# Kernel tuning notes

Measured on AMD Instinct MI355X. Metric: run time of the kernel, lower is better.

Reference implementation:

```python
import jax, jax.numpy as jnp
import numpy as np

EPS_COS = 1e-8
EPS_SHARP = 1e-16


def setup_inputs() -> dict:
    key = jax.random.key(0)
    k1, k2, k3, k4 = jax.random.split(key, 4)
    B, H, R, C, M = 512, 512, 2048, 64, 3
    out_dim = 3 * C + 2 * M + 4  # 202
    h = jax.random.normal(k1, (B, H), dtype=jnp.float32)
    prev_w = jax.random.uniform(k2, (B, R), dtype=jnp.float32)
    prev_w = prev_w / prev_w.sum(axis=1, keepdims=True)  # valid focus distribution
    memory = jax.random.normal(k3, (B, R, C), dtype=jnp.float32)
    fc_w = jax.random.normal(k4, (out_dim, H), dtype=jnp.float32) * 0.05
    fc_b = jnp.zeros((out_dim,), dtype=jnp.float32)
    return {"h": h, "prev_w": prev_w, "memory": memory, "fc_w": fc_w, "fc_b": fc_b}


def _write_head(h, prev_w, memory, fc_w, fc_b):
    B, R, C = memory.shape
    total = fc_w.shape[0]
    shift_len = total - 3 * C - 3          # 2*max_shift + 1
    m = (shift_len - 1) // 2               # max_shift

    z = h @ fc_w.T + fc_b                  # [B, total]
    sizes = [C, 1, 1, shift_len, 1, C, C]
    offs = np.cumsum([0] + sizes)
    k     = jnp.tanh(z[:, offs[0]:offs[1]])                 # [B, C]
    beta  = jax.nn.softplus(z[:, offs[1]:offs[2]])          # [B, 1]
    g     = jax.nn.sigmoid(z[:, offs[2]:offs[3]])           # [B, 1]
    s     = jax.nn.softmax(z[:, offs[3]:offs[4]], axis=1)   # [B, 2m+1]
    gamma = jax.nn.softplus(z[:, offs[4]:offs[5]]) + 1.0    # [B, 1]
    e     = jax.nn.sigmoid(z[:, offs[5]:offs[6]])           # [B, C]
    a     = jnp.tanh(z[:, offs[6]:offs[7]])                 # [B, C]

    # content addressing: cosine similarity of k vs each memory row
    num = jnp.einsum('bc,brc->br', k, memory)
    k_n = jnp.maximum(jnp.linalg.norm(k, axis=1, keepdims=True), EPS_COS)   # [B,1]
    m_n = jnp.maximum(jnp.linalg.norm(memory, axis=2), EPS_COS)             # [B,R]
    w_c = jax.nn.softmax(beta * (num / (k_n * m_n)), axis=1)                # [B,R]

    # gated interpolation
    w_g = g * w_c + (1.0 - g) * prev_w                                      # [B,R]

    # circular shift (per-sample cross-correlation, O(B*R*(2m+1)))
    unrolled = jnp.concatenate([w_g[:, -m:], w_g, w_g[:, :m]], axis=1)      # [B, R+2m]
    windows = jnp.stack([unrolled[:, j:j + R] for j in range(2 * m + 1)], axis=1)  # [B,2m+1,R]
    w_s = jnp.einsum('bjr,bj->br', windows, s)                              # [B,R]

    # sharpen
    w_p = jnp.power(w_s, gamma)
    w = w_p / (w_p.sum(axis=1, keepdims=True) + EPS_SHARP)                  # [B,R]

    # erase + write (fused)
    wE = w[:, :, None]                                                      # [B,R,1]
    new_mem = memory * (1.0 - wE * e[:, None, :]) + wE * a[:, None, :]      # [B,R,C]
    return w, new_mem


def reference(h, prev_w, memory, fc_w, fc_b):
    return _write_head(h, prev_w, memory, fc_w, fc_b)
```

## Files before the change

### kernel.cpp

```cpp
#include <hip/hip_runtime.h>
#include <math.h>

#define BB 512
#define HH 512
#define RR 2048
#define CC 64
#define OUTD 202
#define PSTRIDE 208
#define K_OFF 0
#define E_OFF 64
#define A_OFF 128
#define S_OFF 192
#define COMBO_OFF 199
#define G_OFF 200
#define GAMMA_OFF 201

typedef float f32x4 __attribute__((ext_vector_type(4)));

__device__ __forceinline__ float softplusf_(float x) {
    return (x > 20.f) ? x : log1pf(expf(x));
}
__device__ __forceinline__ float sigmoidf_(float x) {
    return 1.f / (1.f + expf(-x));
}

__global__ __launch_bounds__(256) void params_kernel(
    const float* __restrict__ h, const float* __restrict__ fc_w,
    const float* __restrict__ fc_b, float* __restrict__ pw)
{
    __shared__ float h_sh[8][HH];
    __shared__ float z_sh[8][204];
    const int tid = threadIdx.x;
    const int b0 = blockIdx.x * 8;

    for (int idx = tid; idx < 8 * HH; idx += 256) {
        int j = idx >> 9, i = idx & 511;
        h_sh[j][i] = h[(size_t)(b0 + j) * HH + i];
    }
    __syncthreads();

    if (tid < OUTD) {
        float acc[8];
        #pragma unroll
        for (int j = 0; j < 8; ++j) acc[j] = 0.f;
        const float4* wr4 = (const float4*)(fc_w + (size_t)tid * HH);
        for (int i4 = 0; i4 < HH / 4; ++i4) {
            float4 wv = wr4[i4];
            int i = i4 * 4;
            #pragma unroll
            for (int j = 0; j < 8; ++j) {
                acc[j] = fmaf(wv.x, h_sh[j][i + 0], acc[j]);
                acc[j] = fmaf(wv.y, h_sh[j][i + 1], acc[j]);
                acc[j] = fmaf(wv.z, h_sh[j][i + 2], acc[j]);
                acc[j] = fmaf(wv.w, h_sh[j][i + 3], acc[j]);
            }
        }
        float bias = fc_b[tid];
        #pragma unroll
        for (int j = 0; j < 8; ++j) z_sh[j][tid] = acc[j] + bias;
    }
    __syncthreads();

    for (int idx = tid; idx < 8 * OUTD; idx += 256) {
        int j = idx / OUTD;
        int t = idx - j * OUTD;
        float z = z_sh[j][t];
        float* p = pw + (size_t)(b0 + j) * PSTRIDE;
        if (t < 64)            p[K_OFF + t] = tanhf(z);
        else if (t == 65)      p[G_OFF] = sigmoidf_(z);
        else if (t == 73)      p[GAMMA_OFF] = softplusf_(z) + 1.f;
        else if (t >= 74 && t < 138) p[E_OFF + (t - 74)] = sigmoidf_(z);
        else if (t >= 138)     p[A_OFF + (t - 138)] = tanhf(z);
    }
    __syncthreads();

    if (tid < 8) {
        int j = tid;
        float* p = pw + (size_t)(b0 + j) * PSTRIDE;
        float ss = 0.f;
        for (int c = 0; c < 64; ++c) {
            float kv = tanhf(z_sh[j][c]);
            ss += kv * kv;
        }
        float kn = fmaxf(sqrtf(ss), 1e-8f);
        float beta = softplusf_(z_sh[j][64]);
        p[COMBO_OFF] = beta / kn;
        float mx = -1e30f;
        for (int q = 0; q < 7; ++q) mx = fmaxf(mx, z_sh[j][66 + q]);
        float ev[7], se = 0.f;
        for (int q = 0; q < 7; ++q) { ev[q] = expf(z_sh[j][66 + q] - mx); se += ev[q]; }
        float inv = 1.f / se;
        for (int q = 0; q < 7; ++q) p[S_OFF + q] = ev[q] * inv;
    }
}

__global__ __launch_bounds__(256) void score_kernel(
    const float* __restrict__ memory, const float* __restrict__ pw,
    float* __restrict__ sc)
{
    const int tid = threadIdx.x;
    const int b = blockIdx.x >> 2;
    const int rbase = (blockIdx.x & 3) * 512;
    const int lane16 = tid & 15;
    const int rgrp = tid >> 4;
    const float* p = pw + (size_t)b * PSTRIDE;
    const float4 k4 = *(const float4*)(p + K_OFF + lane16 * 4);
    const float* memb = memory + (size_t)b * RR * CC;

    #pragma unroll 4
    for (int i = 0; i < 32; ++i) {
        int r = rbase + i * 16 + rgrp;
        float4 m4 = *(const float4*)(memb + (size_t)r * CC + lane16 * 4);
        float num = m4.x * k4.x + m4.y * k4.y + m4.z * k4.z + m4.w * k4.w;
        float ssq = m4.x * m4.x + m4.y * m4.y + m4.z * m4.z + m4.w * m4.w;
        #pragma unroll
        for (int m = 1; m < 16; m <<= 1) {
            num += __shfl_xor(num, m, 64);
            ssq += __shfl_xor(ssq, m, 64);
        }
        if (lane16 == 0)
            sc[(size_t)b * RR + r] = num / fmaxf(sqrtf(ssq), 1e-8f);
    }
}

__device__ __forceinline__ float block_reduce_sum256(float v, float* red) {
    #pragma unroll
    for (int m = 1; m < 64; m <<= 1) v += __shfl_xor(v, m, 64);
    int wid = threadIdx.x >> 6;
    if ((threadIdx.x & 63) == 0) red[wid] = v;
    __syncthreads();
    float x = red[0] + red[1] + red[2] + red[3];
    __syncthreads();
    return x;
}

__global__ __launch_bounds__(256) void weight_kernel(
    const float* __restrict__ sc, const float* __restrict__ prev_w,
    const float* __restrict__ pw, float* __restrict__ out_w)
{
    __shared__ float buf[RR];
    __shared__ float wg[RR];
    __shared__ float red[4];
    const int b = blockIdx.x;
    const int tid = threadIdx.x;
    const float* p = pw + (size_t)b * PSTRIDE;
    const float combo = p[COMBO_OFF];
    const float g = p[G_OFF];
    const float gamma = p[GAMMA_OFF];
    const float s0 = p[S_OFF + 0], s1 = p[S_OFF + 1], s2 = p[S_OFF + 2],
                s3 = p[S_OFF + 3], s4 = p[S_OFF + 4], s5 = p[S_OFF + 5],
                s6 = p[S_OFF + 6];

    float ls = 0.f;
    for (int r = tid; r < RR; r += 256) {
        float ev = expf(combo * sc[(size_t)b * RR + r]);
        buf[r] = ev;
        ls += ev;
    }
    const float se = block_reduce_sum256(ls, red);
    const float invse = 1.f / se;

    for (int r = tid; r < RR; r += 256) {
        wg[r] = g * (buf[r] * invse) + (1.f - g) * prev_w[(size_t)b * RR + r];
    }
    __syncthreads();

    float lp = 0.f;
    for (int r = tid; r < RR; r += 256) {
        float acc = s0 * wg[(r - 3) & (RR - 1)]
                  + s1 * wg[(r - 2) & (RR - 1)]
                  + s2 * wg[(r - 1) & (RR - 1)]
                  + s3 * wg[r]
                  + s4 * wg[(r + 1) & (RR - 1)]
                  + s5 * wg[(r + 2) & (RR - 1)]
                  + s6 * wg[(r + 3) & (RR - 1)];
        float wp = powf(acc, gamma);
        buf[r] = wp;
        lp += wp;
    }
    const float ps = block_reduce_sum256(lp, red);
    const float invp = 1.f / (ps + 1e-16f);

    for (int r = tid; r < RR; r += 256) {
        out_w[(size_t)b * RR + r] = buf[r] * invp;
    }
}

__global__ __launch_bounds__(256) void update_kernel(
    const float* __restrict__ memory, const float* __restrict__ w,
    const float* __restrict__ pw, float* __restrict__ out_mem)
{
    const size_t N4 = (size_t)BB * RR * CC / 4;
    const size_t stride = (size_t)2048 * 256;
    const f32x4* m4p = (const f32x4*)memory;
    f32x4* o4p = (f32x4*)out_mem;

    #pragma unroll 2
    for (size_t idx = (size_t)blockIdx.x * 256 + threadIdx.x; idx < N4;
         idx += stride) {
        int br = (int)(idx >> 4);
        int b  = (int)(idx >> 15);
        int c4 = (int)(idx & 15);
        const float* p = pw + (size_t)b * PSTRIDE;
        float wv = w[br];
        f32x4 e4 = *(const f32x4*)(p + E_OFF + c4 * 4);
        f32x4 a4 = *(const f32x4*)(p + A_OFF + c4 * 4);
        f32x4 m4 = m4p[idx];
        f32x4 o;
        o.x = m4.x * (1.f - wv * e4.x) + wv * a4.x;
        o.y = m4.y * (1.f - wv * e4.y) + wv * a4.y;
        o.z = m4.z * (1.f - wv * e4.z) + wv * a4.z;
        o.w = m4.w * (1.f - wv * e4.w) + wv * a4.w;
        __builtin_nontemporal_store(o, &o4p[idx]);
    }
}

extern "C" void kernel_launch(void* const* d_in, const int* in_sizes, int n_in,
                              void* d_out, int out_size, void* d_ws, size_t ws_size,
                              hipStream_t stream) {
    const float* h      = (const float*)d_in[0];
    const float* prev_w = (const float*)d_in[1];
    const float* memory = (const float*)d_in[2];
    const float* fc_w   = (const float*)d_in[3];
    const float* fc_b   = (const float*)d_in[4];

    float* pw      = (float*)d_ws;
    float* out_w   = (float*)d_out;
    float* out_mem = out_w + (size_t)BB * RR;
    float* sc      = out_mem;

    params_kernel<<<64, 256, 0, stream>>>(h, fc_w, fc_b, pw);
    score_kernel<<<BB * 4, 256, 0, stream>>>(memory, pw, sc);
    weight_kernel<<<BB, 256, 0, stream>>>(sc, prev_w, pw, out_w);
    update_kernel<<<2048, 256, 0, stream>>>(memory, out_w, pw, out_mem);
}
```

Before: 209.6 us.

## Move softmax exp into score kernel and reverse-order update for cache reuse

Computes exp(combo*cosine) in the score kernel so the weight kernel only sums and normalizes, and switches powf to the fast __powf. The update kernel becomes per-(batch,row-block) with reversed block order, so the memory slices most recently read by the score kernel are likely still in cache, and loads become nontemporal. It also raises the unroll factor. Risks include lower precision from the fast exp/pow intrinsics and no softmax max-subtraction, which is safe only while cosine times beta stays bounded.

```diff
diff --git a/kernel.cpp b/kernel.cpp
--- a/kernel.cpp
+++ b/kernel.cpp
@@ -105,9 +105,10 @@
     const int rgrp = tid >> 4;
     const float* p = pw + (size_t)b * PSTRIDE;
     const float4 k4 = *(const float4*)(p + K_OFF + lane16 * 4);
+    const float combo = p[COMBO_OFF];
     const float* memb = memory + (size_t)b * RR * CC;
 
-    #pragma unroll 4
+    #pragma unroll 8
     for (int i = 0; i < 32; ++i) {
         int r = rbase + i * 16 + rgrp;
         float4 m4 = *(const float4*)(memb + (size_t)r * CC + lane16 * 4);
@@ -118,8 +119,10 @@
             num += __shfl_xor(num, m, 64);
             ssq += __shfl_xor(ssq, m, 64);
         }
-        if (lane16 == 0)
-            sc[(size_t)b * RR + r] = num / fmaxf(sqrtf(ssq), 1e-8f);
+        if (lane16 == 0) {
+            float mn = fmaxf(sqrtf(ssq), 1e-8f);
+            sc[(size_t)b * RR + r] = __expf(combo * num / mn);
+        }
     }
 }
 
@@ -144,7 +147,6 @@
     const int b = blockIdx.x;
     const int tid = threadIdx.x;
     const float* p = pw + (size_t)b * PSTRIDE;
-    const float combo = p[COMBO_OFF];
     const float g = p[G_OFF];
     const float gamma = p[GAMMA_OFF];
     const float s0 = p[S_OFF + 0], s1 = p[S_OFF + 1], s2 = p[S_OFF + 2],
@@ -153,7 +155,7 @@
 
     float ls = 0.f;
     for (int r = tid; r < RR; r += 256) {
-        float ev = expf(combo * sc[(size_t)b * RR + r]);
+        float ev = sc[(size_t)b * RR + r];
         buf[r] = ev;
         ls += ev;
     }
@@ -174,7 +176,7 @@
                   + s4 * wg[(r + 1) & (RR - 1)]
                   + s5 * wg[(r + 2) & (RR - 1)]
                   + s6 * wg[(r + 3) & (RR - 1)];
-        float wp = powf(acc, gamma);
+        float wp = __powf(acc, gamma);
         buf[r] = wp;
         lp += wp;
     }
@@ -190,28 +192,31 @@
     const float* __restrict__ memory, const float* __restrict__ w,
     const float* __restrict__ pw, float* __restrict__ out_mem)
 {
-    const size_t N4 = (size_t)BB * RR * CC / 4;
-    const size_t stride = (size_t)2048 * 256;
-    const f32x4* m4p = (const f32x4*)memory;
-    f32x4* o4p = (f32x4*)out_mem;
-
-    #pragma unroll 2
-    for (size_t idx = (size_t)blockIdx.x * 256 + threadIdx.x; idx < N4;
-         idx += stride) {
-        int br = (int)(idx >> 4);
-        int b  = (int)(idx >> 15);
-        int c4 = (int)(idx & 15);
-        const float* p = pw + (size_t)b * PSTRIDE;
-        float wv = w[br];
-        f32x4 e4 = *(const f32x4*)(p + E_OFF + c4 * 4);
-        f32x4 a4 = *(const f32x4*)(p + A_OFF + c4 * 4);
-        f32x4 m4 = m4p[idx];
+    const int bid = (int)gridDim.x - 1 - (int)blockIdx.x;
+    const int b = bid >> 2;
+    const int rbase = (bid & 3) * 512;
+    const int tid = threadIdx.x;
+    const int lane16 = tid & 15;
+    const int rgrp = tid >> 4;
+    const float* p = pw + (size_t)b * PSTRIDE;
+    const f32x4 e4 = *(const f32x4*)(p + E_OFF + lane16 * 4);
+    const f32x4 a4 = *(const f32x4*)(p + A_OFF + lane16 * 4);
+    const float* memb = memory + (size_t)b * RR * CC;
+    float* omb = out_mem + (size_t)b * RR * CC;
+    const float* wb = w + (size_t)b * RR;
+
+    #pragma unroll 8
+    for (int i = 0; i < 32; ++i) {
+        int r = rbase + i * 16 + rgrp;
+        float wv = wb[r];
+        const f32x4* mp = (const f32x4*)(memb + (size_t)r * CC) + lane16;
+        f32x4 m4 = __builtin_nontemporal_load(mp);
         f32x4 o;
         o.x = m4.x * (1.f - wv * e4.x) + wv * a4.x;
         o.y = m4.y * (1.f - wv * e4.y) + wv * a4.y;
         o.z = m4.z * (1.f - wv * e4.z) + wv * a4.z;
         o.w = m4.w * (1.f - wv * e4.w) + wv * a4.w;
-        __builtin_nontemporal_store(o, &o4p[idx]);
+        __builtin_nontemporal_store(o, (f32x4*)(omb + (size_t)r * CC) + lane16);
     }
 }
 
@@ -232,5 +237,5 @@
     params_kernel<<<64, 256, 0, stream>>>(h, fc_w, fc_b, pw);
     score_kernel<<<BB * 4, 256, 0, stream>>>(memory, pw, sc);
     weight_kernel<<<BB, 256, 0, stream>>>(sc, prev_w, pw, out_w);
-    update_kernel<<<2048, 256, 0, stream>>>(memory, out_w, pw, out_mem);
-}
+    update_kernel<<<BB * 4, 256, 0, stream>>>(memory, out_w, pw, out_mem);
+}
```

New measurement: 199.1 us. 5.0% less time.
